# Optimization experiments

Hardware: AMD Instinct MI355X
Metric: run time of the kernel (lower is better)

## Reference

```python
import jax, jax.numpy as jnp
import numpy as np
from jax.scipy.linalg import expm

DIM = 1024
N_ROT = 3


def setup_inputs() -> dict:
    key = jax.random.key(0)
    k1, k2 = jax.random.split(key)
    x = jax.random.normal(k1, (4, 4096, DIM), dtype=jnp.float32)
    # raw parameter tensors; skew-symmetrization (as in reset_parameters) done in reference
    generators = jax.random.normal(k2, (N_ROT, DIM, DIM), dtype=jnp.float32) * 0.02
    return {"x": x, "generators": generators}


def reference(x, generators):
    # skew-symmetrize each generator: G <- 0.5*(G - G^T)
    gens = 0.5 * (generators - jnp.swapaxes(generators, -1, -2))
    # sequential rotations: x = x @ expm(G_i) for each of the N_ROT generators
    for i in range(N_ROT):
        rot = expm(gens[i])  # [DIM, DIM] orthogonal rotation
        x = x @ rot
    return x
```

## Files before the change

### kernel.cpp

```cpp
#include <hip/hip_runtime.h>

#define S 1048576
typedef unsigned short u16;
typedef unsigned int u32;
typedef __attribute__((ext_vector_type(8))) short s8v;
typedef __attribute__((ext_vector_type(4))) float f4v;

__device__ __forceinline__ float bf2f(u16 u){
    union { float f; u32 u; } v; v.u = ((u32)u) << 16; return v.f;
}
__device__ __forceinline__ u16 f2bf(float x){
    u32 u = __float_as_uint(x);
    u32 r = (u + 0x7FFFu + ((u >> 16) & 1u)) >> 16;
    return (u16)r;
}
__device__ __forceinline__ void splitf(float x, u16& h, u16& l){
    h = f2bf(x);
    l = f2bf(x - bf2f(h));
}
__device__ __forceinline__ float pairf(const u16* H, const u16* L, size_t off){
    return bf2f(H[off]) + bf2f(L[off]);
}
__device__ __forceinline__ int sidx(int r, int c){ return (r<<6) + (((c) ^ (r&7))<<3); }
__device__ __forceinline__ void gl16(const void* g, void* l){
    __builtin_amdgcn_global_load_lds((const __attribute__((address_space(1))) void*)g,
                                     (__attribute__((address_space(3))) void*)l, 16, 0, 0);
}

__global__ __launch_bounds__(256) void pre_k(const float* __restrict__ G, u16* __restrict__ Abase){
    __shared__ float Gt[64][65];
    const int bid = blockIdx.x;
    const int t = threadIdx.x;
    const int bx = bid & 15, by = (bid >> 4) & 15, z = bid >> 8;
    const float* Gz = G + (size_t)z*S;
    u16* Ah = Abase + (size_t)z*2*S;
    u16* Al = Ah + S;
    const int row = t >> 2, cq = (t & 3) << 4;
    const int r0 = by << 6, c0 = bx << 6;
    #pragma unroll
    for (int g = 0; g < 4; ++g){
        float4 v = *(const float4*)(Gz + (size_t)(c0+row)*1024 + r0 + cq + g*4);
        Gt[row][cq+g*4+0]=v.x; Gt[row][cq+g*4+1]=v.y; Gt[row][cq+g*4+2]=v.z; Gt[row][cq+g*4+3]=v.w;
    }
    __syncthreads();
    #pragma unroll
    for (int g = 0; g < 2; ++g){
        const float* p = Gz + (size_t)(r0+row)*1024 + c0 + cq + g*8;
        float4 v0 = *(const float4*)(p);
        float4 v1 = *(const float4*)(p+4);
        float xs[8] = {v0.x,v0.y,v0.z,v0.w,v1.x,v1.y,v1.z,v1.w};
        s8v sh, sl;
        #pragma unroll
        for (int i = 0; i < 8; ++i){
            float gt = Gt[cq + g*8 + i][row];
            u16 h,l; splitf(0.5f*(xs[i]-gt), h, l);
            sh[i] = (short)h; sl[i] = (short)l;
        }
        *(s8v*)(Ah + (size_t)(r0+row)*1024 + c0 + cq + g*8) = sh;
        *(s8v*)(Al + (size_t)(r0+row)*1024 + c0 + cq + g*8) = sl;
    }
}

template<int MODE, bool XFUSE>
__global__ __launch_bounds__(256) void gemm64_k(const u16* __restrict__ Abase, const u16* __restrict__ Btbase,
                                                u16* __restrict__ Cbase,
                                                const u16* __restrict__ Pab, const u16* __restrict__ Pa2b,
                                                u16* __restrict__ O2base, u16* __restrict__ E2t,
                                                const float* __restrict__ X, u16* __restrict__ Xh,
                                                int u0, int u1){
    __shared__ u16 lds[4*8192];
    const int t = threadIdx.x;
    if (XFUSE && blockIdx.x >= 16){
        const int nb = (int)gridDim.x - 16;
        const int e = ((int)(blockIdx.z*gridDim.y + blockIdx.y))*nb + ((int)blockIdx.x - 16);
        const int E = nb*(int)gridDim.y*(int)gridDim.z;
        for (int u = u0 + e; u < u1; u += E){
            const size_t idx8 = (size_t)u*2048 + (size_t)t*8;
            float4 v0 = *(const float4*)(X+idx8);
            float4 v1 = *(const float4*)(X+idx8+4);
            float xs[8] = {v0.x,v0.y,v0.z,v0.w,v1.x,v1.y,v1.z,v1.w};
            s8v h;
            #pragma unroll
            for (int i = 0; i < 8; ++i) h[i] = (short)f2bf(xs[i]);
            *(s8v*)(Xh+idx8) = h;
        }
        return;
    }
    const int z = blockIdx.z;
    const u16* Ah = Abase  + (size_t)z*2*S;
    const u16* Bh = Btbase + (size_t)z*2*S; const u16* Bl = Bh + S;
    u16* Ch = Cbase + (size_t)z*2*S;
    const u16* Pah = Pab + (size_t)z*2*S;   const u16* Pal = Pah + S;
    const u16* P2h = Pa2b + (size_t)z*2*S;
    u16* O2h = O2base + (size_t)z*2*S;
    const int brow = blockIdx.y << 6, bcol = blockIdx.x << 6;
    const int lane = t & 63, w = t >> 6;
    const int wm = (w >> 1) << 5, wn = (w & 1) << 5;
    const int lr = lane & 15, g = lane >> 4;
    int qq[2]; size_t goA[2], goB[2];
    #pragma unroll
    for (int i = 0; i < 2; ++i){
        int q = (((w<<1)+i)<<6) + lane;
        int r = q >> 3, c = lane & 7;
        qq[i] = q << 3;
        goA[i] = (size_t)(brow+r)*1024 + ((c^(r&7))<<3);
        goB[i] = (size_t)(bcol+r)*1024 + ((c^(r&7))<<3);
    }
    auto issue = [&](int kt){
        u16* L = lds + (kt & 3) * 8192;
        const int k0 = kt << 6;
        #pragma unroll
        for (int i = 0; i < 2; ++i){
            gl16(Ah + goA[i] + k0, L + qq[i]);
            gl16(Bh + goB[i] + k0, L + 4096 + qq[i]);
        }
    };
    issue(0); issue(1); issue(2);
    f4v acc[2][2] = {};
    for (int kt = 0; kt < 16; ++kt){
        if (kt <= 13)      asm volatile("s_waitcnt vmcnt(8)" ::: "memory");
        else if (kt == 14) asm volatile("s_waitcnt vmcnt(4)" ::: "memory");
        else               asm volatile("s_waitcnt vmcnt(0)" ::: "memory");
        __builtin_amdgcn_s_barrier();
        __builtin_amdgcn_sched_barrier(0);
        if (kt <= 12) issue(kt + 3);
        const u16* L = lds + (kt & 3) * 8192;
        #pragma unroll
        for (int ks = 0; ks < 2; ++ks){
            const int ch = (ks << 2) + g;
            s8v a_h[2], b_h[2];
            #pragma unroll
            for (int f = 0; f < 2; ++f){
                const int ra = wm+(f<<4)+lr, rb = wn+(f<<4)+lr;
                a_h[f] = *(const s8v*)&L[sidx(ra,ch)];
                b_h[f] = *(const s8v*)&L[4096 + sidx(rb,ch)];
            }
            __builtin_amdgcn_s_setprio(1);
            #pragma unroll
            for (int mf = 0; mf < 2; ++mf)
                #pragma unroll
                for (int nf = 0; nf < 2; ++nf)
                    acc[mf][nf] = __builtin_amdgcn_mfma_f32_16x16x32_bf16(a_h[mf], b_h[nf], acc[mf][nf], 0,0,0);
            __builtin_amdgcn_s_setprio(0);
        }
    }
    const int orr = g << 2;
    #pragma unroll
    for (int mf = 0; mf < 2; ++mf)
        #pragma unroll
        for (int nf = 0; nf < 2; ++nf)
            #pragma unroll
            for (int r = 0; r < 4; ++r){
                const int orow = brow + wm + (mf<<4) + orr + r;
                const int ocol = bcol + wn + (nf<<4) + lr;
                const size_t off = (size_t)orow*1024 + ocol;
                const float av = acc[mf][nf][r];
                if (MODE == 0){
                    Ch[off] = f2bf(av);
                }
                if (MODE == 1){
                    Ch[off] = f2bf(av);
                    float a = pairf(Bh, Bl, off);
                    O2h[off] = f2bf((1.0f/6.0f)*a - (1.0f/24.0f)*av);
                }
                if (MODE == 2){
                    float a  = pairf(Pah, Pal, off);
                    float a2 = bf2f(P2h[off]);
                    float e = a - 0.5f*a2 - av + (orow == ocol ? 1.0f : 0.0f);
                    u16 h = f2bf(e);
                    O2h[off] = h;
                    if (z == 2) E2t[(size_t)ocol*1024 + orow] = h;
                }
            }
}

__global__ __launch_bounds__(512) void gemm_big3(const u16* __restrict__ Xh, const u16* __restrict__ Rth,
                                                 float* __restrict__ Y){
    __shared__ u16 lds[2][32768];
    const int bid = blockIdx.x;
    const int swz = (bid & 7)*32 + (bid >> 3);
    const int by = swz >> 2, bx = swz & 3;
    const int brow = by << 8, bcol = bx << 8;
    const int t = threadIdx.x;
    const int lane = t & 63, w = t >> 6;
    const int wm = (w >> 2) << 7, wn = (w & 3) << 6;
    const int lr = lane & 15, g = lane >> 4;
    int xq[4]; size_t gx[4], gb[4];
    #pragma unroll
    for (int i = 0; i < 4; ++i){
        int q = (((w<<2)+i)<<6) + lane;
        int r = q >> 3, c = lane & 7;
        xq[i] = q << 3;
        gx[i] = (size_t)(brow+r)*1024 + ((c^(r&7))<<3);
        gb[i] = (size_t)(bcol+r)*1024 + ((c^(r&7))<<3);
    }
    f4v acc[8][4] = {};
    {
        u16* L = lds[0];
        #pragma unroll
        for (int i = 0; i < 4; ++i){
            gl16(Xh  + gx[i], L + xq[i]);
            gl16(Rth + gb[i], L + 16384 + xq[i]);
        }
    }
    int cur = 0;
    for (int kt = 0; kt < 16; ++kt){
        __syncthreads();
        if (kt < 15){
            u16* L = lds[cur^1];
            const int k0 = (kt+1) << 6;
            #pragma unroll
            for (int i = 0; i < 4; ++i){
                gl16(Xh  + gx[i] + k0, L + xq[i]);
                gl16(Rth + gb[i] + k0, L + 16384 + xq[i]);
            }
        }
        const u16* L = lds[cur];
        #pragma unroll
        for (int ks = 0; ks < 2; ++ks){
            const int ch = (ks << 2) + g;
            s8v bh[4];
            #pragma unroll
            for (int nf = 0; nf < 4; ++nf){
                const int rb = wn+(nf<<4)+lr;
                bh[nf] = *(const s8v*)&L[16384 + sidx(rb,ch)];
            }
            __builtin_amdgcn_s_setprio(1);
            #pragma unroll
            for (int mf = 0; mf < 8; ++mf){
                const int ra = wm+(mf<<4)+lr;
                s8v a = *(const s8v*)&L[sidx(ra,ch)];
                #pragma unroll
                for (int nf = 0; nf < 4; ++nf)
                    acc[mf][nf] = __builtin_amdgcn_mfma_f32_16x16x32_bf16(a, bh[nf], acc[mf][nf], 0,0,0);
            }
            __builtin_amdgcn_s_setprio(0);
        }
        cur ^= 1;
    }
    const int orr = g << 2;
    #pragma unroll
    for (int mf = 0; mf < 8; ++mf)
        #pragma unroll
        for (int nf = 0; nf < 4; ++nf)
            #pragma unroll
            for (int r = 0; r < 4; ++r){
                int orow = brow + wm + (mf<<4) + orr + r;
                int ocol = bcol + wn + (nf<<4) + lr;
                Y[(size_t)orow*1024 + ocol] = acc[mf][nf][r];
            }
}

__global__ __launch_bounds__(256) void gemm_big_f(const float* __restrict__ Xv, const u16* __restrict__ Rth,
                                                  float* __restrict__ Y){
    __shared__ u16 Xs[128*64], Bhs[128*64];
    const int bid = blockIdx.x;
    const int swz = (bid & 7)*128 + (bid >> 3);
    const int bx = swz & 7, by = swz >> 3;
    const int brow = by << 7, bcol = bx << 7;
    const int t = threadIdx.x;
    const int sr = t >> 1, cb = (t & 1) << 2;
    const int lane = t & 63, w = t >> 6;
    const int wm = (w >> 1) << 6, wn = (w & 1) << 6;
    const int lr = lane & 15, g = lane >> 4;
    s8v xr[4], bhr[4];
    auto load_tile = [&](int k0){
        #pragma unroll
        for (int i = 0; i < 4; ++i){
            const size_t bo = (size_t)(bcol+sr)*1024 + k0 + ((cb+i)<<3);
            bhr[i] = *(const s8v*)(Rth + bo);
        }
        #pragma unroll
        for (int i = 0; i < 4; ++i){
            const float* p = Xv + (size_t)(brow+sr)*1024 + k0 + ((cb+i)<<3);
            float4 f0 = *(const float4*)(p), f1 = *(const float4*)(p+4);
            float xs[8] = {f0.x,f0.y,f0.z,f0.w,f1.x,f1.y,f1.z,f1.w};
            #pragma unroll
            for (int j = 0; j < 8; ++j) xr[i][j] = (short)f2bf(xs[j]);
        }
    };
    load_tile(0);
    f4v acc[4][4] = {};
    for (int k0 = 0; k0 < 1024; k0 += 64){
        __syncthreads();
        #pragma unroll
        for (int i = 0; i < 4; ++i){
            const int si = sidx(sr, cb+i);
            *(s8v*)&Xs[si]  = xr[i];
            *(s8v*)&Bhs[si] = bhr[i];
        }
        __syncthreads();
        if (k0 < 960) load_tile(k0 + 64);
        #pragma unroll
        for (int ks = 0; ks < 2; ++ks){
            const int ch = (ks << 2) + g;
            s8v bhf[4];
            #pragma unroll
            for (int nf = 0; nf < 4; ++nf)
                bhf[nf] = *(const s8v*)&Bhs[sidx(wn+(nf<<4)+lr, ch)];
            #pragma unroll
            for (int mf = 0; mf < 4; ++mf){
                s8v ah = *(const s8v*)&Xs[sidx(wm+(mf<<4)+lr, ch)];
                #pragma unroll
                for (int nf = 0; nf < 4; ++nf)
                    acc[mf][nf] = __builtin_amdgcn_mfma_f32_16x16x32_bf16(ah, bhf[nf], acc[mf][nf], 0,0,0);
            }
        }
    }
    const int orr = g << 2;
    #pragma unroll
    for (int mf = 0; mf < 4; ++mf)
        #pragma unroll
        for (int nf = 0; nf < 4; ++nf)
            #pragma unroll
            for (int r = 0; r < 4; ++r){
                int orow = brow + wm + (mf<<4) + orr + r;
                int ocol = bcol + wn + (nf<<4) + lr;
                Y[(size_t)orow*1024 + ocol] = acc[mf][nf][r];
            }
}

extern "C" void kernel_launch(void* const* d_in, const int* in_sizes, int n_in,
                              void* d_out, int out_size, void* d_ws, size_t ws_size,
                              hipStream_t stream) {
    const float* X = (const float*)d_in[0];
    const float* G = (const float*)d_in[1];
    float* out = (float*)d_out;
    u16* ob = (u16*)d_out;
    auto slot = [&](int i){ return ob + (size_t)i*2*S; };
    u16* RT = (u16*)d_ws;
    u16* Xh = RT + (size_t)2*S;
    const bool ws_ok = ws_size >= (size_t)36*S;

    dim3 b(256);
    pre_k<<<dim3(768), b, 0, stream>>>(G, slot(0));
    if (ws_ok){
        gemm64_k<1,true><<<dim3(32,16,3), b, 0, stream>>>(slot(0), slot(0), slot(3),
                                                          slot(0), slot(0), slot(6), slot(15),
                                                          X, Xh, 0, 4096);
        gemm64_k<2,true><<<dim3(32,16,3), b, 0, stream>>>(slot(6), slot(3), slot(14),
                                                          slot(0), slot(3), slot(9), slot(15),
                                                          X, Xh, 4096, 8192);
    } else {
        gemm64_k<1,false><<<dim3(16,16,3), b, 0, stream>>>(slot(0), slot(0), slot(3),
                                                           slot(0), slot(0), slot(6), slot(15),
                                                           X, Xh, 0, 0);
        gemm64_k<2,false><<<dim3(16,16,3), b, 0, stream>>>(slot(6), slot(3), slot(14),
                                                           slot(0), slot(3), slot(9), slot(15),
                                                           X, Xh, 0, 0);
    }
    gemm64_k<0,false><<<dim3(16,16,1), b, 0, stream>>>(slot(15), slot(10), slot(12),
                                                       slot(0), slot(0), slot(12), slot(15),
                                                       X, Xh, 0, 0);
    gemm64_k<0,false><<<dim3(16,16,1), b, 0, stream>>>(slot(12), slot(9), RT,
                                                       slot(0), slot(0), RT, slot(15),
                                                       X, Xh, 0, 0);
    if (ws_ok)
        gemm_big3<<<dim3(256), dim3(512), 0, stream>>>(Xh, RT, out);
    else
        gemm_big_f<<<dim3(1024), b, 0, stream>>>(X, RT, out);
}
```

Before: 124.1 us.

## Rebalance X bf16 conversion across pre_k and MODE0 gemms; shrink LDS pipeline

Moves the fp32-to-bf16 conversion of X out of the 3-batch MODE1/MODE2 gemms and into extra blocks of pre_k and the two single-batch MODE0 gemms. Those gemms launch only 256 tiles and so leave most CUs idle. The gemm64 LDS ring drops from 4 stages to 3 with prefetch depth 2, which lowers shared-memory use. Non-fused launches also get a block-index swizzle meant to improve L2 locality. The cost is shallower latency hiding in the K loop.

```diff
diff --git a/kernel.cpp b/kernel.cpp
--- a/kernel.cpp
+++ b/kernel.cpp
@@ -26,11 +26,26 @@
     __builtin_amdgcn_global_load_lds((const __attribute__((address_space(1))) void*)g,
                                      (__attribute__((address_space(3))) void*)l, 16, 0, 0);
 }
-
-__global__ __launch_bounds__(256) void pre_k(const float* __restrict__ G, u16* __restrict__ Abase){
+__device__ __forceinline__ void xconv1(const float* __restrict__ X, u16* __restrict__ Xh, int u, int t){
+    const size_t idx8 = (size_t)u*2048 + (size_t)t*8;
+    float4 v0 = *(const float4*)(X+idx8);
+    float4 v1 = *(const float4*)(X+idx8+4);
+    float xs[8] = {v0.x,v0.y,v0.z,v0.w,v1.x,v1.y,v1.z,v1.w};
+    s8v h;
+    #pragma unroll
+    for (int i = 0; i < 8; ++i) h[i] = (short)f2bf(xs[i]);
+    *(s8v*)(Xh+idx8) = h;
+}
+
+__global__ __launch_bounds__(256) void pre_k(const float* __restrict__ G, u16* __restrict__ Abase,
+                                             const float* __restrict__ X, u16* __restrict__ Xh){
     __shared__ float Gt[64][65];
     const int bid = blockIdx.x;
     const int t = threadIdx.x;
+    if (bid >= 768){
+        for (int u = bid - 768; u < 2731; u += 1024) xconv1(X, Xh, u, t);
+        return;
+    }
     const int bx = bid & 15, by = (bid >> 4) & 15, z = bid >> 8;
     const float* Gz = G + (size_t)z*S;
     u16* Ah = Abase + (size_t)z*2*S;
@@ -68,32 +83,30 @@
                                                 u16* __restrict__ O2base, u16* __restrict__ E2t,
                                                 const float* __restrict__ X, u16* __restrict__ Xh,
                                                 int u0, int u1){
-    __shared__ u16 lds[4*8192];
+    __shared__ u16 lds[3*8192];
     const int t = threadIdx.x;
     if (XFUSE && blockIdx.x >= 16){
         const int nb = (int)gridDim.x - 16;
         const int e = ((int)(blockIdx.z*gridDim.y + blockIdx.y))*nb + ((int)blockIdx.x - 16);
         const int E = nb*(int)gridDim.y*(int)gridDim.z;
-        for (int u = u0 + e; u < u1; u += E){
-            const size_t idx8 = (size_t)u*2048 + (size_t)t*8;
-            float4 v0 = *(const float4*)(X+idx8);
-            float4 v1 = *(const float4*)(X+idx8+4);
-            float xs[8] = {v0.x,v0.y,v0.z,v0.w,v1.x,v1.y,v1.z,v1.w};
-            s8v h;
-            #pragma unroll
-            for (int i = 0; i < 8; ++i) h[i] = (short)f2bf(xs[i]);
-            *(s8v*)(Xh+idx8) = h;
-        }
+        for (int u = u0 + e; u < u1; u += E) xconv1(X, Xh, u, t);
         return;
     }
     const int z = blockIdx.z;
+    int bx, by;
+    if (XFUSE){ bx = blockIdx.x; by = blockIdx.y; }
+    else {
+        const int lin = (int)blockIdx.x + ((int)blockIdx.y << 4);
+        const int sw = (lin & 7)*32 + (lin >> 3);
+        bx = sw & 15; by = sw >> 4;
+    }
     const u16* Ah = Abase  + (size_t)z*2*S;
     const u16* Bh = Btbase + (size_t)z*2*S; const u16* Bl = Bh + S;
     u16* Ch = Cbase + (size_t)z*2*S;
     const u16* Pah = Pab + (size_t)z*2*S;   const u16* Pal = Pah + S;
     const u16* P2h = Pa2b + (size_t)z*2*S;
     u16* O2h = O2base + (size_t)z*2*S;
-    const int brow = blockIdx.y << 6, bcol = blockIdx.x << 6;
+    const int brow = by << 6, bcol = bx << 6;
     const int lane = t & 63, w = t >> 6;
     const int wm = (w >> 1) << 5, wn = (w & 1) << 5;
     const int lr = lane & 15, g = lane >> 4;
@@ -107,7 +120,7 @@
         goB[i] = (size_t)(bcol+r)*1024 + ((c^(r&7))<<3);
     }
     auto issue = [&](int kt){
-        u16* L = lds + (kt & 3) * 8192;
+        u16* L = lds + (kt % 3) * 8192;
         const int k0 = kt << 6;
         #pragma unroll
         for (int i = 0; i < 2; ++i){
@@ -115,16 +128,15 @@
             gl16(Bh + goB[i] + k0, L + 4096 + qq[i]);
         }
     };
-    issue(0); issue(1); issue(2);
+    issue(0); issue(1);
     f4v acc[2][2] = {};
     for (int kt = 0; kt < 16; ++kt){
-        if (kt <= 13)      asm volatile("s_waitcnt vmcnt(8)" ::: "memory");
-        else if (kt == 14) asm volatile("s_waitcnt vmcnt(4)" ::: "memory");
-        else               asm volatile("s_waitcnt vmcnt(0)" ::: "memory");
+        if (kt < 15) asm volatile("s_waitcnt vmcnt(4)" ::: "memory");
+        else         asm volatile("s_waitcnt vmcnt(0)" ::: "memory");
         __builtin_amdgcn_s_barrier();
         __builtin_amdgcn_sched_barrier(0);
-        if (kt <= 12) issue(kt + 3);
-        const u16* L = lds + (kt & 3) * 8192;
+        if (kt < 14) issue(kt + 2);
+        const u16* L = lds + (kt % 3) * 8192;
         #pragma unroll
         for (int ks = 0; ks < 2; ++ks){
             const int ch = (ks << 2) + g;
@@ -333,30 +345,28 @@
     const bool ws_ok = ws_size >= (size_t)36*S;
 
     dim3 b(256);
-    pre_k<<<dim3(768), b, 0, stream>>>(G, slot(0));
+    pre_k<<<dim3(ws_ok ? 1792 : 768), b, 0, stream>>>(G, slot(0), X, Xh);
+    gemm64_k<1,false><<<dim3(16,16,3), b, 0, stream>>>(slot(0), slot(0), slot(3),
+                                                       slot(0), slot(0), slot(6), slot(15),
+                                                       X, Xh, 0, 0);
+    gemm64_k<2,false><<<dim3(16,16,3), b, 0, stream>>>(slot(6), slot(3), slot(14),
+                                                       slot(0), slot(3), slot(9), slot(15),
+                                                       X, Xh, 0, 0);
     if (ws_ok){
-        gemm64_k<1,true><<<dim3(32,16,3), b, 0, stream>>>(slot(0), slot(0), slot(3),
-                                                          slot(0), slot(0), slot(6), slot(15),
-                                                          X, Xh, 0, 4096);
-        gemm64_k<2,true><<<dim3(32,16,3), b, 0, stream>>>(slot(6), slot(3), slot(14),
-                                                          slot(0), slot(3), slot(9), slot(15),
-                                                          X, Xh, 4096, 8192);
+        gemm64_k<0,true><<<dim3(64,16,1), b, 0, stream>>>(slot(15), slot(10), slot(12),
+                                                          slot(0), slot(0), slot(12), slot(15),
+                                                          X, Xh, 2731, 5462);
+        gemm64_k<0,true><<<dim3(64,16,1), b, 0, stream>>>(slot(12), slot(9), RT,
+                                                          slot(0), slot(0), RT, slot(15),
+                                                          X, Xh, 5462, 8192);
+        gemm_big3<<<dim3(256), dim3(512), 0, stream>>>(Xh, RT, out);
     } else {
-        gemm64_k<1,false><<<dim3(16,16,3), b, 0, stream>>>(slot(0), slot(0), slot(3),
-                                                           slot(0), slot(0), slot(6), slot(15),
+        gemm64_k<0,false><<<dim3(16,16,1), b, 0, stream>>>(slot(15), slot(10), slot(12),
+                                                           slot(0), slot(0), slot(12), slot(15),
                                                            X, Xh, 0, 0);
-        gemm64_k<2,false><<<dim3(16,16,3), b, 0, stream>>>(slot(6), slot(3), slot(14),
-                                                           slot(0), slot(3), slot(9), slot(15),
+        gemm64_k<0,false><<<dim3(16,16,1), b, 0, stream>>>(slot(12), slot(9), RT,
+                                                           slot(0), slot(0), RT, slot(15),
                                                            X, Xh, 0, 0);
-    }
-    gemm64_k<0,false><<<dim3(16,16,1), b, 0, stream>>>(slot(15), slot(10), slot(12),
-                                                       slot(0), slot(0), slot(12), slot(15),
-                                                       X, Xh, 0, 0);
-    gemm64_k<0,false><<<dim3(16,16,1), b, 0, stream>>>(slot(12), slot(9), RT,
-                                                       slot(0), slot(0), RT, slot(15),
-                                                       X, Xh, 0, 0);
-    if (ws_ok)
-        gemm_big3<<<dim3(256), dim3(512), 0, stream>>>(Xh, RT, out);
-    else
         gemm_big_f<<<dim3(1024), b, 0, stream>>>(X, RT, out);
-}
+    }
+}
```

Result: faster. 115.4 us (-7.0%).
